# Optimization experiments

Hardware: AMD Instinct MI355X
Metric: run time of the kernel (lower is better)

Reference implementation:

```python
import jax, jax.numpy as jnp
import numpy as np

N = 8192
IN_DIM = 256
HID = 512
NUM_CLASSES = 256
AVG_DEG = 32


def setup_inputs() -> dict:
    key = jax.random.key(0)
    k_a, k_x, k_w1, k_w2 = jax.random.split(key, 4)
    # Binary adjacency with avg degree ~AVG_DEG (entries are exactly 1.0, matching
    # A.nonzero() edge extraction with implicit unit edge weights).
    A = (jax.random.uniform(k_a, (N, N)) < (AVG_DEG / N)).astype(jnp.float32)
    x = jax.random.normal(k_x, (N, IN_DIM), dtype=jnp.float32)
    # GCNConv params: glorot-ish weights, zero bias.
    W1 = jax.random.normal(k_w1, (IN_DIM, HID), dtype=jnp.float32) / np.sqrt(IN_DIM)
    b1 = jnp.zeros((HID,), dtype=jnp.float32)
    W2 = jax.random.normal(k_w2, (HID, NUM_CLASSES), dtype=jnp.float32) / np.sqrt(HID)
    b2 = jnp.zeros((NUM_CLASSES,), dtype=jnp.float32)
    sigmoid_param = jnp.array([10.0], dtype=jnp.float32)
    return {"A": A, "x": x, "W1": W1, "b1": b1, "W2": W2, "b2": b2,
            "sigmoid_param": sigmoid_param}


def _gcn_propagate(A, deg_inv_sqrt, h):
    # PyG GCNConv aggregation with self-loops, without materializing A + I:
    # out_j = d_j^{-1/2} * sum_i A_ij d_i^{-1/2} h_i  +  d_j^{-1} h_j
    m = deg_inv_sqrt[:, None] * h              # [N, d]
    agg = A.T @ m                              # messages flow row -> col
    return deg_inv_sqrt[:, None] * agg + (deg_inv_sqrt[:, None] ** 2) * h


def reference(A, x, W1, b1, W2, b2, sigmoid_param):
    # Degree from column sums of (A + I) — matches gcn_norm's scatter on col.
    deg = jnp.sum(A, axis=0) + 1.0             # [N], >= 1 thanks to self-loop
    deg_inv_sqrt = jax.lax.rsqrt(deg)
    skip_x = x                                  # nn.Identity skip connection
    # GCNConv 1: linear then normalized aggregation, then bias; ReLU.
    h = _gcn_propagate(A, deg_inv_sqrt, x @ W1) + b1
    h = jax.nn.relu(h)
    # GCNConv 2.
    h = _gcn_propagate(A, deg_inv_sqrt, h @ W2) + b2
    # Skip add + scaled sigmoid (original casts to double; kept float32 here).
    return jax.nn.sigmoid(sigmoid_param * (h + skip_x))
```

## Files before the change

### kernel.cpp

```cpp
#include <hip/hip_runtime.h>
#include <hip/hip_bf16.h>

#define N_NODES 8192
#define IN_DIM  256
#define HID     512
#define NCLS    256
#define CAP     128

typedef __attribute__((ext_vector_type(8))) __bf16 bf16x8;
typedef __attribute__((ext_vector_type(4))) float  floatx4;

static __device__ __forceinline__ float bf2f(ushort u) {
    union { float f; unsigned int i; } v; v.i = ((unsigned int)u) << 16; return v.f;
}
static __device__ __forceinline__ ushort f2bf(float f) {
    __hip_bfloat16 b = __float2bfloat16(f);
    return *reinterpret_cast<ushort*>(&b);
}

__global__ __launch_bounds__(256) void build_csc(const float* __restrict__ A,
                                                 int* __restrict__ col_cnt,
                                                 int* __restrict__ col_idx) {
    const int jbase = (blockIdx.x * 256 + threadIdx.x) * 4;
    const int i0 = blockIdx.y * 32;
    for (int ii = 0; ii < 32; ++ii) {
        const int i = i0 + ii;
        float4 v = *reinterpret_cast<const float4*>(A + (size_t)i * N_NODES + jbase);
        if (v.x != 0.0f) { int p = atomicAdd(&col_cnt[jbase + 0], 1); if (p < CAP) col_idx[(size_t)(jbase + 0) * CAP + p] = i; }
        if (v.y != 0.0f) { int p = atomicAdd(&col_cnt[jbase + 1], 1); if (p < CAP) col_idx[(size_t)(jbase + 1) * CAP + p] = i; }
        if (v.z != 0.0f) { int p = atomicAdd(&col_cnt[jbase + 2], 1); if (p < CAP) col_idx[(size_t)(jbase + 2) * CAP + p] = i; }
        if (v.w != 0.0f) { int p = atomicAdd(&col_cnt[jbase + 3], 1); if (p < CAP) col_idx[(size_t)(jbase + 3) * CAP + p] = i; }
    }
}

__global__ __launch_bounds__(256) void prep_w(const float* __restrict__ W1,
                                              const float* __restrict__ W2,
                                              ushort* __restrict__ W1Th, ushort* __restrict__ W1Tl,
                                              ushort* __restrict__ W2Th, ushort* __restrict__ W2Tl) {
    const int idx = blockIdx.x * 256 + threadIdx.x;
    {
        const int k = idx / HID, n = idx % HID;
        const float v = W1[idx]; const ushort h = f2bf(v);
        W1Th[(size_t)n * IN_DIM + k] = h;
        W1Tl[(size_t)n * IN_DIM + k] = f2bf(v - bf2f(h));
    }
    {
        const int k = idx / NCLS, n = idx % NCLS;
        const float v = W2[idx]; const ushort h = f2bf(v);
        W2Th[(size_t)n * HID + k] = h;
        W2Tl[(size_t)n * HID + k] = f2bf(v - bf2f(h));
    }
}

__global__ __launch_bounds__(256) void agg_x(const float* __restrict__ x,
                                             const int* __restrict__ col_idx,
                                             const int* __restrict__ col_cnt,
                                             ushort* __restrict__ px_hi,
                                             ushort* __restrict__ px_lo) {
    const int j = blockIdx.x;
    const int d = threadIdx.x;
    const int cntj = min(col_cnt[j], CAP);
    const float dj = rsqrtf((float)col_cnt[j] + 1.0f);
    float acc = dj * x[(size_t)j * IN_DIM + d];
    const int* __restrict__ lst = col_idx + (size_t)j * CAP;
    int e = 0;
    for (; e + 3 < cntj; e += 4) {
        const int i0 = lst[e], i1 = lst[e + 1], i2 = lst[e + 2], i3 = lst[e + 3];
        const float d0 = rsqrtf((float)col_cnt[i0] + 1.0f);
        const float d1 = rsqrtf((float)col_cnt[i1] + 1.0f);
        const float d2 = rsqrtf((float)col_cnt[i2] + 1.0f);
        const float d3 = rsqrtf((float)col_cnt[i3] + 1.0f);
        const float v0 = x[(size_t)i0 * IN_DIM + d];
        const float v1 = x[(size_t)i1 * IN_DIM + d];
        const float v2 = x[(size_t)i2 * IN_DIM + d];
        const float v3 = x[(size_t)i3 * IN_DIM + d];
        acc += d0 * v0 + d1 * v1 + d2 * v2 + d3 * v3;
    }
    for (; e < cntj; ++e) {
        const int i = lst[e];
        acc += rsqrtf((float)col_cnt[i] + 1.0f) * x[(size_t)i * IN_DIM + d];
    }
    acc *= dj;
    const ushort hi = f2bf(acc);
    px_hi[(size_t)j * IN_DIM + d] = hi;
    px_lo[(size_t)j * IN_DIM + d] = f2bf(acc - bf2f(hi));
}

__device__ __forceinline__ void gemm_core(const ushort* __restrict__ Ah,
                                          const ushort* __restrict__ Al,
                                          const ushort* __restrict__ Bh,
                                          const ushort* __restrict__ Bl,
                                          int K, int m_base, int n_base,
                                          int l16, int quad, floatx4 acc[4][2]) {
    for (int k0 = 0; k0 < K; k0 += 32) {
        const int kf = k0 + quad * 8;
        bf16x8 ah[4], al[4], bh[2], bl[2];
#pragma unroll
        for (int t = 0; t < 4; ++t) {
            const size_t ao = (size_t)(m_base + t * 16 + l16) * K + kf;
            ah[t] = *reinterpret_cast<const bf16x8*>(Ah + ao);
            al[t] = *reinterpret_cast<const bf16x8*>(Al + ao);
        }
#pragma unroll
        for (int t = 0; t < 2; ++t) {
            const size_t bo = (size_t)(n_base + t * 16 + l16) * K + kf;
            bh[t] = *reinterpret_cast<const bf16x8*>(Bh + bo);
            bl[t] = *reinterpret_cast<const bf16x8*>(Bl + bo);
        }
#pragma unroll
        for (int tm = 0; tm < 4; ++tm)
#pragma unroll
            for (int tn = 0; tn < 2; ++tn) {
                acc[tm][tn] = __builtin_amdgcn_mfma_f32_16x16x32_bf16(ah[tm], bl[tn], acc[tm][tn], 0, 0, 0);
                acc[tm][tn] = __builtin_amdgcn_mfma_f32_16x16x32_bf16(al[tm], bh[tn], acc[tm][tn], 0, 0, 0);
                acc[tm][tn] = __builtin_amdgcn_mfma_f32_16x16x32_bf16(ah[tm], bh[tn], acc[tm][tn], 0, 0, 0);
            }
    }
}

__global__ __launch_bounds__(256) void gemm1_fused(const ushort* __restrict__ Ah,
                                                   const ushort* __restrict__ Al,
                                                   const ushort* __restrict__ Bh,
                                                   const ushort* __restrict__ Bl,
                                                   const float* __restrict__ b1,
                                                   ushort* __restrict__ h_hi,
                                                   ushort* __restrict__ h_lo) {
    const int tid = threadIdx.x;
    const int lane = tid & 63, wave = tid >> 6;
    const int wm = wave >> 1, wn = wave & 1;
    const int l16 = lane & 15, quad = lane >> 4;
    const int m_base = blockIdx.x * 128 + wm * 64;
    const int n_base = blockIdx.y * 64 + wn * 32;
    floatx4 acc[4][2] = {};
    gemm_core(Ah, Al, Bh, Bl, IN_DIM, m_base, n_base, l16, quad, acc);
#pragma unroll
    for (int tn = 0; tn < 2; ++tn) {
        const int col = n_base + tn * 16 + l16;
        const float bv = b1[col];
#pragma unroll
        for (int tm = 0; tm < 4; ++tm)
#pragma unroll
            for (int r = 0; r < 4; ++r) {
                const int row = m_base + tm * 16 + quad * 4 + r;
                const float v = fmaxf(acc[tm][tn][r] + bv, 0.0f);
                const ushort hi = f2bf(v);
                h_hi[(size_t)row * HID + col] = hi;
                h_lo[(size_t)row * HID + col] = f2bf(v - bf2f(hi));
            }
    }
}

__global__ __launch_bounds__(256) void gemm2(const ushort* __restrict__ Ah,
                                             const ushort* __restrict__ Al,
                                             const ushort* __restrict__ Bh,
                                             const ushort* __restrict__ Bl,
                                             float* __restrict__ C) {
    const int tid = threadIdx.x;
    const int lane = tid & 63, wave = tid >> 6;
    const int wm = wave >> 1, wn = wave & 1;
    const int l16 = lane & 15, quad = lane >> 4;
    const int m_base = blockIdx.x * 128 + wm * 64;
    const int n_base = blockIdx.y * 64 + wn * 32;
    floatx4 acc[4][2] = {};
    gemm_core(Ah, Al, Bh, Bl, HID, m_base, n_base, l16, quad, acc);
#pragma unroll
    for (int tm = 0; tm < 4; ++tm)
#pragma unroll
        for (int tn = 0; tn < 2; ++tn)
#pragma unroll
            for (int r = 0; r < 4; ++r)
                C[(size_t)(m_base + tm * 16 + quad * 4 + r) * NCLS + (n_base + tn * 16 + l16)] = acc[tm][tn][r];
}

__global__ __launch_bounds__(256) void agg_out(const float* __restrict__ g2,
                                               const int* __restrict__ col_idx,
                                               const int* __restrict__ col_cnt,
                                               const float* __restrict__ b2,
                                               const float* __restrict__ x,
                                               const float* __restrict__ sp_p,
                                               float* __restrict__ out) {
    const int j = blockIdx.x;
    const int d = threadIdx.x;
    const int cntj = min(col_cnt[j], CAP);
    const float dj = rsqrtf((float)col_cnt[j] + 1.0f);
    float acc = dj * g2[(size_t)j * NCLS + d];
    const int* __restrict__ lst = col_idx + (size_t)j * CAP;
    int e = 0;
    for (; e + 3 < cntj; e += 4) {
        const int i0 = lst[e], i1 = lst[e + 1], i2 = lst[e + 2], i3 = lst[e + 3];
        const float d0 = rsqrtf((float)col_cnt[i0] + 1.0f);
        const float d1 = rsqrtf((float)col_cnt[i1] + 1.0f);
        const float d2 = rsqrtf((float)col_cnt[i2] + 1.0f);
        const float d3 = rsqrtf((float)col_cnt[i3] + 1.0f);
        const float v0 = g2[(size_t)i0 * NCLS + d];
        const float v1 = g2[(size_t)i1 * NCLS + d];
        const float v2 = g2[(size_t)i2 * NCLS + d];
        const float v3 = g2[(size_t)i3 * NCLS + d];
        acc += d0 * v0 + d1 * v1 + d2 * v2 + d3 * v3;
    }
    for (; e < cntj; ++e) {
        const int i = lst[e];
        acc += rsqrtf((float)col_cnt[i] + 1.0f) * g2[(size_t)i * NCLS + d];
    }
    const float sp = sp_p[0];
    const float val = dj * acc + b2[d] + x[(size_t)j * NCLS + d];
    out[(size_t)j * NCLS + d] = 1.0f / (1.0f + __expf(-sp * val));
}

extern "C" void kernel_launch(void* const* d_in, const int* in_sizes, int n_in,
                              void* d_out, int out_size, void* d_ws, size_t ws_size,
                              hipStream_t stream) {
    const float* A  = (const float*)d_in[0];
    const float* x  = (const float*)d_in[1];
    const float* W1 = (const float*)d_in[2];
    const float* b1 = (const float*)d_in[3];
    const float* W2 = (const float*)d_in[4];
    const float* b2 = (const float*)d_in[5];
    const float* sp = (const float*)d_in[6];
    float* out = (float*)d_out;

    char* ws = (char*)d_ws;
    size_t off = 0;
    auto alloc = [&](size_t bytes) {
        void* p = ws + off;
        off = (off + bytes + 255) & ~(size_t)255;
        return p;
    };
    int*    col_cnt = (int*)   alloc((size_t)N_NODES * 4);
    int*    col_idx = (int*)   alloc((size_t)N_NODES * CAP * 4);
    ushort* px_hi   = (ushort*)alloc((size_t)N_NODES * IN_DIM * 2);
    ushort* px_lo   = (ushort*)alloc((size_t)N_NODES * IN_DIM * 2);
    ushort* W1Th    = (ushort*)alloc((size_t)HID * IN_DIM * 2);
    ushort* W1Tl    = (ushort*)alloc((size_t)HID * IN_DIM * 2);
    ushort* W2Th    = (ushort*)alloc((size_t)NCLS * HID * 2);
    ushort* W2Tl    = (ushort*)alloc((size_t)NCLS * HID * 2);
    ushort* h_hi    = (ushort*)alloc((size_t)N_NODES * HID * 2);
    ushort* h_lo    = (ushort*)alloc((size_t)N_NODES * HID * 2);
    float*  g2      = (float*) alloc((size_t)N_NODES * NCLS * 4);

    hipMemsetAsync(col_cnt, 0, (size_t)N_NODES * 4, stream);

    build_csc<<<dim3(8, 256), 256, 0, stream>>>(A, col_cnt, col_idx);
    prep_w<<<(IN_DIM * HID) / 256, 256, 0, stream>>>(W1, W2, W1Th, W1Tl, W2Th, W2Tl);

    agg_x<<<N_NODES, 256, 0, stream>>>(x, col_idx, col_cnt, px_hi, px_lo);
    gemm1_fused<<<dim3(N_NODES / 128, HID / 64), 256, 0, stream>>>(
        px_hi, px_lo, W1Th, W1Tl, b1, h_hi, h_lo);

    gemm2<<<dim3(N_NODES / 128, NCLS / 64), 256, 0, stream>>>(
        h_hi, h_lo, W2Th, W2Tl, g2);
    agg_out<<<N_NODES, 256, 0, stream>>>(g2, col_idx, col_cnt, b2, x, sp, out);
}
```

Baseline: 502.4 us.

## Precompute per-edge normalization weights and vectorize aggregation with one wave per node

Adds kernels that compute each node's inverse-sqrt degree once and store per-edge neighbor weights. This removes the repeated col_cnt gathers and rsqrt work from the aggregation inner loops. The two aggregation kernels now give one 64-lane wave per node, with each lane handling four features through float4 loads and stores, so each block covers four nodes. The cost is two extra small launches and an extra 4 MB weight array.

```diff
diff --git a/kernel.cpp b/kernel.cpp
--- a/kernel.cpp
+++ b/kernel.cpp
@@ -33,6 +33,21 @@
     }
 }
 
+__global__ __launch_bounds__(256) void compute_dis(const int* __restrict__ col_cnt,
+                                                   float* __restrict__ dis) {
+    const int j = blockIdx.x * 256 + threadIdx.x;
+    dis[j] = rsqrtf((float)col_cnt[j] + 1.0f);
+}
+
+__global__ __launch_bounds__(128) void fill_w(const int* __restrict__ col_idx,
+                                              const int* __restrict__ col_cnt,
+                                              const float* __restrict__ dis,
+                                              float* __restrict__ w) {
+    const int j = blockIdx.x, e = threadIdx.x;
+    if (e < min(col_cnt[j], CAP))
+        w[(size_t)j * CAP + e] = dis[col_idx[(size_t)j * CAP + e]];
+}
+
 __global__ __launch_bounds__(256) void prep_w(const float* __restrict__ W1,
                                               const float* __restrict__ W2,
                                               ushort* __restrict__ W1Th, ushort* __restrict__ W1Tl,
@@ -55,35 +70,42 @@
 __global__ __launch_bounds__(256) void agg_x(const float* __restrict__ x,
                                              const int* __restrict__ col_idx,
                                              const int* __restrict__ col_cnt,
+                                             const float* __restrict__ dis,
+                                             const float* __restrict__ w,
                                              ushort* __restrict__ px_hi,
                                              ushort* __restrict__ px_lo) {
-    const int j = blockIdx.x;
-    const int d = threadIdx.x;
-    const int cntj = min(col_cnt[j], CAP);
-    const float dj = rsqrtf((float)col_cnt[j] + 1.0f);
-    float acc = dj * x[(size_t)j * IN_DIM + d];
-    const int* __restrict__ lst = col_idx + (size_t)j * CAP;
+    const int j = __builtin_amdgcn_readfirstlane(blockIdx.x * 4 + (threadIdx.x >> 6));
+    const int d = (threadIdx.x & 63) * 4;
+    const int cnt = min(col_cnt[j], CAP);
+    const float dj = dis[j];
+    const float4 self = *reinterpret_cast<const float4*>(x + (size_t)j * IN_DIM + d);
+    float ax = dj * self.x, ay = dj * self.y, az = dj * self.z, aw = dj * self.w;
+    const int*   __restrict__ lst = col_idx + (size_t)j * CAP;
+    const float* __restrict__ wl  = w       + (size_t)j * CAP;
     int e = 0;
-    for (; e + 3 < cntj; e += 4) {
+    for (; e + 4 <= cnt; e += 4) {
         const int i0 = lst[e], i1 = lst[e + 1], i2 = lst[e + 2], i3 = lst[e + 3];
-        const float d0 = rsqrtf((float)col_cnt[i0] + 1.0f);
-        const float d1 = rsqrtf((float)col_cnt[i1] + 1.0f);
-        const float d2 = rsqrtf((float)col_cnt[i2] + 1.0f);
-        const float d3 = rsqrtf((float)col_cnt[i3] + 1.0f);
-        const float v0 = x[(size_t)i0 * IN_DIM + d];
-        const float v1 = x[(size_t)i1 * IN_DIM + d];
-        const float v2 = x[(size_t)i2 * IN_DIM + d];
-        const float v3 = x[(size_t)i3 * IN_DIM + d];
-        acc += d0 * v0 + d1 * v1 + d2 * v2 + d3 * v3;
-    }
-    for (; e < cntj; ++e) {
+        const float w0 = wl[e], w1 = wl[e + 1], w2 = wl[e + 2], w3 = wl[e + 3];
+        const float4 v0 = *reinterpret_cast<const float4*>(x + (size_t)i0 * IN_DIM + d);
+        const float4 v1 = *reinterpret_cast<const float4*>(x + (size_t)i1 * IN_DIM + d);
+        const float4 v2 = *reinterpret_cast<const float4*>(x + (size_t)i2 * IN_DIM + d);
+        const float4 v3 = *reinterpret_cast<const float4*>(x + (size_t)i3 * IN_DIM + d);
+        ax += w0 * v0.x + w1 * v1.x + w2 * v2.x + w3 * v3.x;
+        ay += w0 * v0.y + w1 * v1.y + w2 * v2.y + w3 * v3.y;
+        az += w0 * v0.z + w1 * v1.z + w2 * v2.z + w3 * v3.z;
+        aw += w0 * v0.w + w1 * v1.w + w2 * v2.w + w3 * v3.w;
+    }
+    for (; e < cnt; ++e) {
         const int i = lst[e];
-        acc += rsqrtf((float)col_cnt[i] + 1.0f) * x[(size_t)i * IN_DIM + d];
-    }
-    acc *= dj;
-    const ushort hi = f2bf(acc);
-    px_hi[(size_t)j * IN_DIM + d] = hi;
-    px_lo[(size_t)j * IN_DIM + d] = f2bf(acc - bf2f(hi));
+        const float we = wl[e];
+        const float4 v = *reinterpret_cast<const float4*>(x + (size_t)i * IN_DIM + d);
+        ax += we * v.x; ay += we * v.y; az += we * v.z; aw += we * v.w;
+    }
+    ax *= dj; ay *= dj; az *= dj; aw *= dj;
+    const ushort hx = f2bf(ax), hy = f2bf(ay), hz = f2bf(az), hw = f2bf(aw);
+    *reinterpret_cast<ushort4*>(px_hi + (size_t)j * IN_DIM + d) = ushort4{hx, hy, hz, hw};
+    *reinterpret_cast<ushort4*>(px_lo + (size_t)j * IN_DIM + d) =
+        ushort4{f2bf(ax - bf2f(hx)), f2bf(ay - bf2f(hy)), f2bf(az - bf2f(hz)), f2bf(aw - bf2f(hw))};
 }
 
 __device__ __forceinline__ void gemm_core(const ushort* __restrict__ Ah,
@@ -175,36 +197,48 @@
 __global__ __launch_bounds__(256) void agg_out(const float* __restrict__ g2,
                                                const int* __restrict__ col_idx,
                                                const int* __restrict__ col_cnt,
+                                               const float* __restrict__ dis,
+                                               const float* __restrict__ w,
                                                const float* __restrict__ b2,
                                                const float* __restrict__ x,
                                                const float* __restrict__ sp_p,
                                                float* __restrict__ out) {
-    const int j = blockIdx.x;
-    const int d = threadIdx.x;
-    const int cntj = min(col_cnt[j], CAP);
-    const float dj = rsqrtf((float)col_cnt[j] + 1.0f);
-    float acc = dj * g2[(size_t)j * NCLS + d];
-    const int* __restrict__ lst = col_idx + (size_t)j * CAP;
+    const int j = __builtin_amdgcn_readfirstlane(blockIdx.x * 4 + (threadIdx.x >> 6));
+    const int d = (threadIdx.x & 63) * 4;
+    const int cnt = min(col_cnt[j], CAP);
+    const float dj = dis[j];
+    const float4 self = *reinterpret_cast<const float4*>(g2 + (size_t)j * NCLS + d);
+    float ax = dj * self.x, ay = dj * self.y, az = dj * self.z, aw = dj * self.w;
+    const int*   __restrict__ lst = col_idx + (size_t)j * CAP;
+    const float* __restrict__ wl  = w       + (size_t)j * CAP;
     int e = 0;
-    for (; e + 3 < cntj; e += 4) {
+    for (; e + 4 <= cnt; e += 4) {
         const int i0 = lst[e], i1 = lst[e + 1], i2 = lst[e + 2], i3 = lst[e + 3];
-        const float d0 = rsqrtf((float)col_cnt[i0] + 1.0f);
-        const float d1 = rsqrtf((float)col_cnt[i1] + 1.0f);
-        const float d2 = rsqrtf((float)col_cnt[i2] + 1.0f);
-        const float d3 = rsqrtf((float)col_cnt[i3] + 1.0f);
-        const float v0 = g2[(size_t)i0 * NCLS + d];
-        const float v1 = g2[(size_t)i1 * NCLS + d];
-        const float v2 = g2[(size_t)i2 * NCLS + d];
-        const float v3 = g2[(size_t)i3 * NCLS + d];
-        acc += d0 * v0 + d1 * v1 + d2 * v2 + d3 * v3;
-    }
-    for (; e < cntj; ++e) {
+        const float w0 = wl[e], w1 = wl[e + 1], w2 = wl[e + 2], w3 = wl[e + 3];
+        const float4 v0 = *reinterpret_cast<const float4*>(g2 + (size_t)i0 * NCLS + d);
+        const float4 v1 = *reinterpret_cast<const float4*>(g2 + (size_t)i1 * NCLS + d);
+        const float4 v2 = *reinterpret_cast<const float4*>(g2 + (size_t)i2 * NCLS + d);
+        const float4 v3 = *reinterpret_cast<const float4*>(g2 + (size_t)i3 * NCLS + d);
+        ax += w0 * v0.x + w1 * v1.x + w2 * v2.x + w3 * v3.x;
+        ay += w0 * v0.y + w1 * v1.y + w2 * v2.y + w3 * v3.y;
+        az += w0 * v0.z + w1 * v1.z + w2 * v2.z + w3 * v3.z;
+        aw += w0 * v0.w + w1 * v1.w + w2 * v2.w + w3 * v3.w;
+    }
+    for (; e < cnt; ++e) {
         const int i = lst[e];
-        acc += rsqrtf((float)col_cnt[i] + 1.0f) * g2[(size_t)i * NCLS + d];
+        const float we = wl[e];
+        const float4 v = *reinterpret_cast<const float4*>(g2 + (size_t)i * NCLS + d);
+        ax += we * v.x; ay += we * v.y; az += we * v.z; aw += we * v.w;
     }
     const float sp = sp_p[0];
-    const float val = dj * acc + b2[d] + x[(size_t)j * NCLS + d];
-    out[(size_t)j * NCLS + d] = 1.0f / (1.0f + __expf(-sp * val));
+    const float4 bv = *reinterpret_cast<const float4*>(b2 + d);
+    const float4 xv = *reinterpret_cast<const float4*>(x + (size_t)j * NCLS + d);
+    float4 o;
+    o.x = 1.0f / (1.0f + __expf(-sp * (dj * ax + bv.x + xv.x)));
+    o.y = 1.0f / (1.0f + __expf(-sp * (dj * ay + bv.y + xv.y)));
+    o.z = 1.0f / (1.0f + __expf(-sp * (dj * az + bv.z + xv.z)));
+    o.w = 1.0f / (1.0f + __expf(-sp * (dj * aw + bv.w + xv.w)));
+    *reinterpret_cast<float4*>(out + (size_t)j * NCLS + d) = o;
 }
 
 extern "C" void kernel_launch(void* const* d_in, const int* in_sizes, int n_in,
@@ -227,7 +261,9 @@
         return p;
     };
     int*    col_cnt = (int*)   alloc((size_t)N_NODES * 4);
+    float*  dis     = (float*) alloc((size_t)N_NODES * 4);
     int*    col_idx = (int*)   alloc((size_t)N_NODES * CAP * 4);
+    float*  wedge   = (float*) alloc((size_t)N_NODES * CAP * 4);
     ushort* px_hi   = (ushort*)alloc((size_t)N_NODES * IN_DIM * 2);
     ushort* px_lo   = (ushort*)alloc((size_t)N_NODES * IN_DIM * 2);
     ushort* W1Th    = (ushort*)alloc((size_t)HID * IN_DIM * 2);
@@ -241,13 +277,15 @@
     hipMemsetAsync(col_cnt, 0, (size_t)N_NODES * 4, stream);
 
     build_csc<<<dim3(8, 256), 256, 0, stream>>>(A, col_cnt, col_idx);
+    compute_dis<<<N_NODES / 256, 256, 0, stream>>>(col_cnt, dis);
+    fill_w<<<N_NODES, 128, 0, stream>>>(col_idx, col_cnt, dis, wedge);
     prep_w<<<(IN_DIM * HID) / 256, 256, 0, stream>>>(W1, W2, W1Th, W1Tl, W2Th, W2Tl);
 
-    agg_x<<<N_NODES, 256, 0, stream>>>(x, col_idx, col_cnt, px_hi, px_lo);
+    agg_x<<<N_NODES / 4, 256, 0, stream>>>(x, col_idx, col_cnt, dis, wedge, px_hi, px_lo);
     gemm1_fused<<<dim3(N_NODES / 128, HID / 64), 256, 0, stream>>>(
         px_hi, px_lo, W1Th, W1Tl, b1, h_hi, h_lo);
 
     gemm2<<<dim3(N_NODES / 128, NCLS / 64), 256, 0, stream>>>(
         h_hi, h_lo, W2Th, W2Tl, g2);
-    agg_out<<<N_NODES, 256, 0, stream>>>(g2, col_idx, col_cnt, b2, x, sp, out);
-}
+    agg_out<<<N_NODES / 4, 256, 0, stream>>>(g2, col_idx, col_cnt, dis, wedge, b2, x, sp, out);
+}
```

New measurement: 496.3 us. About the same (-1.2%).
